# Performance work log

Measured on AMD Instinct MI355X. Metric: run time of the kernel, lower is better.

## Reference

```python
import jax, jax.numpy as jnp
import numpy as np

NPOINT, RADIUS, SIGMA, K = 1024, 0.1, 0.05, 32
KDE_K = 128  # N_points default of kernel_density_estimation_ball


def setup_inputs() -> dict:
    key = jax.random.key(0)
    ks = jax.random.split(key, 9)
    B, N, C = 4, 4096, 16

    def glorot(k, shape):
        fan_in, fan_out = shape
        return jax.random.normal(k, shape, jnp.float32) * jnp.sqrt(2.0 / (fan_in + fan_out))

    return {
        'xyz': jax.random.uniform(ks[0], (B, N, 3), jnp.float32),      # unit cube
        'feature': jax.random.normal(ks[1], (B, N, C), jnp.float32),
        'w_mlp0': glorot(ks[2], (3 + C, 128)),
        'w_mlp1': glorot(ks[3], (128, 128)),
        'w_mlp2': glorot(ks[4], (128, 256)),
        'w_wn': glorot(ks[5], (3, 32)),
        'w_nl0': glorot(ks[6], (1, 16)),
        'w_nl1': glorot(ks[7], (16, 1)),
        'w_np': glorot(ks[8], (32, 256)),
    }


def _pdist2(a, b):
    # squared pairwise distances [B, M, N]
    return (jnp.sum(a * a, -1)[:, :, None] + jnp.sum(b * b, -1)[:, None, :]
            - 2.0 * jnp.einsum('bmd,bnd->bmn', a, b))


def _fps(xyz, npoint):
    # farthest point sampling, seeded at index 0 (matches CUDA op semantics)
    B, N, _ = xyz.shape

    def step(carry, _):
        min_d, last = carry
        p = jnp.take_along_axis(xyz, last[:, None, None], axis=1)  # [B,1,3]
        d = jnp.sum((xyz - p) ** 2, -1)                            # [B,N]
        min_d = jnp.minimum(min_d, d)
        nxt = jnp.argmax(min_d, axis=1).astype(jnp.int32)
        return (min_d, nxt), nxt

    init = (jnp.full((B, N), jnp.inf, xyz.dtype), jnp.zeros((B,), jnp.int32))
    _, rest = jax.lax.scan(step, init, None, length=npoint - 1)
    return jnp.concatenate([jnp.zeros((B, 1), jnp.int32), rest.T], axis=1)  # [B,npoint]


def _ball_query(xyz, radius, k):
    # first-k-in-index-order neighbors with d2 < r^2, padded with first hit
    B, N, _ = xyz.shape
    d2 = _pdist2(xyz, xyz)
    in_ball = d2 < radius * radius                 # self always included
    j = jnp.arange(N, dtype=jnp.int32)
    keys = jnp.where(in_ball, j, j + N)            # in-ball indices sort first
    _, idx = jax.lax.top_k(-keys, k)               # k smallest keys -> positions j
    cnt = jnp.minimum(jnp.sum(in_ball, axis=-1), k)            # [B,N]
    valid = jnp.arange(k) < cnt[..., None]
    idx = jnp.where(valid, idx, idx[..., :1])
    return idx, cnt


def _kde_ball(xyz, radius, sigma, kde_k):
    idx, cnt = _ball_query(xyz, radius, kde_k)     # [B,N,kde_k], [B,N]
    b_ix = jnp.arange(xyz.shape[0])[:, None, None]
    g = xyz[b_ix, idx] - xyz[:, :, None, :]        # [B,N,kde_k,3]
    R = jnp.sqrt(jnp.float32(sigma))
    quad = jnp.sum(jnp.square(g / R), axis=-1)     # [B,N,kde_k]
    mvn = jnp.exp(-0.5 * quad - 3.0 * jnp.log(R) - 1.5 * jnp.log(2.0 * 3.1415926))
    first = mvn[..., :1]
    total = jnp.sum(mvn, axis=-1, keepdims=True)
    cntf = cnt.astype(xyz.dtype)[..., None]
    total = total - first * (jnp.float32(kde_k) - cntf)  # remove padded duplicates
    return total / cntf                             # [B,N,1]


def _knn(k, src, q):
    d2 = _pdist2(q, src)                            # [B,P,N]
    _, idx = jax.lax.top_k(-d2, k)                  # ascending distance
    return idx


def _forward(xyz, feature, w_mlp0, w_mlp1, w_mlp2, w_wn, w_nl0, w_nl1, w_np):
    B = xyz.shape[0]
    conv = lambda x, w: jax.nn.relu(jnp.einsum('bpkc,cf->bpkf', x, w))  # bias-free 1x1 conv

    fps_idx = _fps(xyz, NPOINT)
    new_xyz = jnp.take_along_axis(xyz, fps_idx[..., None], axis=1)      # [B,P,3]

    knn_idx = _knn(K, xyz, new_xyz)                                      # [B,P,K]
    b_ix = jnp.arange(B)[:, None, None]
    grouped_xyz = xyz[b_ix, knn_idx] - new_xyz[:, :, None, :]            # [B,P,K,3]
    grouped_feature = jnp.concatenate([grouped_xyz, feature[b_ix, knn_idx]], axis=-1)

    inv_density = 1.0 / _kde_ball(xyz, RADIUS, SIGMA, KDE_K)             # [B,N,1]
    grouped_density = inv_density[b_ix, knn_idx]                          # [B,P,K,1]
    density_scale = grouped_density / jnp.max(grouped_density, axis=2, keepdims=True)

    h = conv(conv(conv(grouped_feature, w_mlp0), w_mlp1), w_mlp2)        # [B,P,K,256]
    weight = conv(grouped_xyz, w_wn)                                      # [B,P,K,32]
    density_scale = conv(conv(density_scale, w_nl0), w_nl1)               # [B,P,K,1]

    pts = h * density_scale
    pts = jnp.einsum('bpkc,bpkw->bpcw', pts, weight)                      # [B,P,256,32]
    # np_conv: 1x1 kernel with stride [1, mlp[-1]] + VALID -> only c=0 slice survives
    out = jax.nn.relu(jnp.einsum('bpw,wf->bpf', pts[:, :, 0, :], w_np))   # [B,P,256]
    return new_xyz, out


def reference(xyz, feature, w_mlp0, w_mlp1, w_mlp2, w_wn, w_nl0, w_nl1, w_np):
    return _forward(xyz, feature, w_mlp0, w_mlp1, w_mlp2, w_wn, w_nl0, w_nl1, w_np)
```

## Files before the change

### kernel.cpp

```cpp
#include <hip/hip_runtime.h>
#include <math.h>

#pragma clang fp contract(off)

typedef float v2f __attribute__((ext_vector_type(2)));

__global__ __launch_bounds__(256) void prep_kernel(
    const float* __restrict__ xyz, const float* __restrict__ w0,
    const float* __restrict__ w1, const float* __restrict__ w2,
    float* __restrict__ norms, float* __restrict__ W0T,
    float* __restrict__ W1T, float* __restrict__ W2c)
{
    int t = blockIdx.x * 256 + threadIdx.x;
    if (t < 16384) {
        float x = xyz[t*3+0], y = xyz[t*3+1], z = xyz[t*3+2];
        norms[t] = (x*x + y*y) + z*z;
        int c = t >> 7, k = t & 127;
        W1T[c*128 + k] = w1[k*128 + c];
    }
    if (t < 2432) { int c = t / 19, i = t - c*19; W0T[t] = w0[i*128 + c]; }
    if (t < 128)  { W2c[t] = w2[t*256]; }
}

template<int CTRL>
__device__ __forceinline__ unsigned long long dpp_u64(unsigned long long k) {
    int lo = (int)(unsigned int)k;
    int hi = (int)(unsigned int)(k >> 32);
    int plo = __builtin_amdgcn_update_dpp(lo, lo, CTRL, 0xF, 0xF, false);
    int phi = __builtin_amdgcn_update_dpp(hi, hi, CTRL, 0xF, 0xF, false);
    return ((unsigned long long)(unsigned int)phi << 32) | (unsigned int)plo;
}
template<int CTRL>
__device__ __forceinline__ unsigned long long max_u64_dpp(unsigned long long k) {
    unsigned long long p = dpp_u64<CTRL>(k);
    return p > k ? p : k;
}
template<int CTRL>
__device__ __forceinline__ unsigned long long min_u64_dpp(unsigned long long k) {
    unsigned long long p = dpp_u64<CTRL>(k);
    return p < k ? p : k;
}
__device__ __forceinline__ unsigned long long max_u64(unsigned long long a,
                                                      unsigned long long b) {
    return a > b ? a : b;
}

__global__ __launch_bounds__(512) void fps_kde_kernel(
    const float* __restrict__ xyz, const float* __restrict__ norms,
    float* __restrict__ new_xyz, float* __restrict__ invden)
{
    __shared__ float4 pts[4096];
    __shared__ float  nxb[3072];
    __shared__ __attribute__((aligned(16))) unsigned long long swk[2][32];
    int tid = threadIdx.x;

    if (blockIdx.x < 4) {
        int b = blockIdx.x;
        const float* Xb = xyz + b*12288;
        for (int t = tid; t < 4096; t += 512)
            pts[t] = make_float4(Xb[t*3+0], Xb[t*3+1], Xb[t*3+2], 0.0f);
        __syncthreads();
        float4 P[8];
#pragma unroll
        for (int k = 0; k < 8; ++k) P[k] = pts[k*512 + tid];
        v2f Xp[4], Yp[4], Zp[4], md2[4];
#pragma unroll
        for (int k = 0; k < 4; ++k) {
            Xp[k].x = P[k].x;  Xp[k].y = P[k+4].x;
            Yp[k].x = P[k].y;  Yp[k].y = P[k+4].y;
            Zp[k].x = P[k].z;  Zp[k].y = P[k+4].z;
            md2[k].x = INFINITY; md2[k].y = INFINITY;
        }
        unsigned ip[8];
#pragma unroll
        for (int k = 0; k < 8; ++k) ip[k] = ~((unsigned)(k*512 + tid));
        float cx = pts[0].x, cy = pts[0].y, cz = pts[0].z;
        if (tid == 0) { nxb[0] = cx; nxb[1] = cy; nxb[2] = cz; }
        int buf = 0;
        for (int it = 1; it < 1024; ++it) {
            v2f cx2, cy2, cz2;
            cx2.x = cx; cx2.y = cx;
            cy2.x = cy; cy2.y = cy;
            cz2.x = cz; cz2.y = cz;
#pragma unroll
            for (int k = 0; k < 4; ++k) {
                v2f dx = Xp[k] - cx2, dy = Yp[k] - cy2, dz = Zp[k] - cz2;
                v2f dd = (dx*dx + dy*dy) + dz*dz;
                md2[k].x = fminf(md2[k].x, dd.x);
                md2[k].y = fminf(md2[k].y, dd.y);
            }
            unsigned long long k0 =
                ((unsigned long long)__float_as_uint(md2[0].x) << 32) | ip[0];
            unsigned long long k1 =
                ((unsigned long long)__float_as_uint(md2[1].x) << 32) | ip[1];
            unsigned long long k2 =
                ((unsigned long long)__float_as_uint(md2[2].x) << 32) | ip[2];
            unsigned long long k3 =
                ((unsigned long long)__float_as_uint(md2[3].x) << 32) | ip[3];
            unsigned long long k4 =
                ((unsigned long long)__float_as_uint(md2[0].y) << 32) | ip[4];
            unsigned long long k5 =
                ((unsigned long long)__float_as_uint(md2[1].y) << 32) | ip[5];
            unsigned long long k6 =
                ((unsigned long long)__float_as_uint(md2[2].y) << 32) | ip[6];
            unsigned long long k7 =
                ((unsigned long long)__float_as_uint(md2[3].y) << 32) | ip[7];
            unsigned long long t01 = max_u64(k0, k1);
            unsigned long long t23 = max_u64(k2, k3);
            unsigned long long t45 = max_u64(k4, k5);
            unsigned long long t67 = max_u64(k6, k7);
            unsigned long long t03 = max_u64(t01, t23);
            unsigned long long t47 = max_u64(t45, t67);
            unsigned long long key = max_u64(t03, t47);
            key = max_u64_dpp<0xB1>(key);
            key = max_u64_dpp<0x4E>(key);
            key = max_u64_dpp<0x141>(key);
            key = max_u64_dpp<0x140>(key);
            if ((tid & 15) == 0) swk[buf][tid >> 4] = key;
            __syncthreads();
            uint4 w4 = *((const uint4*)&swk[buf][(tid & 15) << 1]);
            unsigned long long kA = ((unsigned long long)w4.y << 32) | w4.x;
            unsigned long long kB = ((unsigned long long)w4.w << 32) | w4.z;
            unsigned long long kk = kA > kB ? kA : kB;
            kk = max_u64_dpp<0xB1>(kk);
            kk = max_u64_dpp<0x4E>(kk);
            kk = max_u64_dpp<0x141>(kk);
            kk = max_u64_dpp<0x140>(kk);
            int fp = (int)(~(unsigned int)kk);
            float4 c = pts[fp];
            cx = c.x; cy = c.y; cz = c.z;
            if (tid == 0) { nxb[it*3+0] = cx; nxb[it*3+1] = cy; nxb[it*3+2] = cz; }
            buf ^= 1;
        }
        __syncthreads();
        float* NX = new_xyz + b*3072;
        for (int t = tid; t < 3072; t += 512) NX[t] = nxb[t];
    } else {
        int idx = blockIdx.x - 4;
        int b = idx >> 9;
        int wave = tid >> 6, lane = tid & 63;
        int i_local = ((idx & 511) << 3) + wave;
        const float* Xb = xyz + b*12288;
        const float* Nb = norms + b*4096;
        for (int t = tid; t < 4096; t += 512)
            pts[t] = make_float4(Xb[t*3+0], Xb[t*3+1], Xb[t*3+2], Nb[t]);
        __syncthreads();
        float4 c = pts[i_local];
        const float Rv    = sqrtf(0.05f);
        const float inv_s = 1.0f / (Rv*Rv);
        const float K1    = -3.0f*logf(Rv) - 1.5f*logf(2.0f*3.1415926f);
        float csum = 0.0f; int cnt = 0;
        for (int j = lane; j < 4096; j += 64) {
            float4 q = pts[j];
            float dot = (c.x*q.x + c.y*q.y) + c.z*q.z;
            float t2 = 2.0f * dot;
            float d2 = (c.w + q.w) - t2;
            if (d2 < 0.01f) {
                float gx = q.x - c.x, gy = q.y - c.y, gz = q.z - c.z;
                float dd = (gx*gx + gy*gy) + gz*gz;
                csum += expf(-0.5f * (dd * inv_s) + K1);
                cnt  += 1;
            }
        }
#pragma unroll
        for (int m = 1; m < 64; m <<= 1) {
            csum += __shfl_xor(csum, m, 64);
            cnt  += __shfl_xor(cnt,  m, 64);
        }
        if (lane == 0) {
            float den = csum / (float)cnt;
            invden[b*4096 + i_local] = 1.0f / den;
        }
    }
}

__global__ __launch_bounds__(256) void knn_kernel(
    const float* __restrict__ xyz, const float* __restrict__ norms,
    const float* __restrict__ new_xyz, int* __restrict__ knn_idx)
{
    __shared__ unsigned sd2[4*4096];
    __shared__ int sIdx[4*32];
    int wave = threadIdx.x >> 6, lane = threadIdx.x & 63;
    int qg = blockIdx.x*4 + wave;
    int b = qg >> 10;
    const float* Q = new_xyz + qg*3;
    float qx = Q[0], qy = Q[1], qz = Q[2];
    float nq = (qx*qx + qy*qy) + qz*qz;
    const float* Xb = xyz + b*12288;
    const float* Nb = norms + b*4096;
    unsigned* d2w = sd2 + wave*4096;
    for (int j = lane; j < 4096; j += 64) {
        float x = Xb[j*3+0], y = Xb[j*3+1], z = Xb[j*3+2];
        float dot = (qx*x + qy*y) + qz*z;
        float t2 = 2.0f*dot;
        float d = (nq + Nb[j]) - t2;
        unsigned u = __float_as_uint(d);
        unsigned m = ((unsigned)((int)u >> 31)) | 0x80000000u;
        d2w[j] = u ^ m;
    }
    for (int r = 0; r < 32; ++r) {
        unsigned best = 0xFFFFFFFFu; int bj = 0;
#pragma unroll
        for (int t = 0; t < 16; ++t) {
            int jb = t*256 + lane*4;
            uint4 v = *((const uint4*)(d2w + jb));
            if (v.x < best) { best = v.x; bj = jb;   }
            if (v.y < best) { best = v.y; bj = jb+1; }
            if (v.z < best) { best = v.z; bj = jb+2; }
            if (v.w < best) { best = v.w; bj = jb+3; }
        }
        unsigned long long key = ((unsigned long long)best << 32) | (unsigned)bj;
        key = min_u64_dpp<0xB1>(key);
        key = min_u64_dpp<0x4E>(key);
        key = min_u64_dpp<0x141>(key);
        key = min_u64_dpp<0x140>(key);
        key = min_u64_dpp<0x142>(key);
        key = min_u64_dpp<0x143>(key);
        int jwin = __builtin_amdgcn_readlane((int)(unsigned)key, 63);
        if (lane == 0) { sIdx[wave*32 + r] = jwin; d2w[jwin] = 0xFFFFFFFFu; }
    }
    if (lane < 32) knn_idx[qg*32 + lane] = sIdx[wave*32 + lane];
}

__global__ __launch_bounds__(256, 2) void group_mlp_kernel(
    const float* __restrict__ xyz, const float* __restrict__ feat,
    const float* __restrict__ new_xyz, const int* __restrict__ knn_idx,
    const float* __restrict__ invden,
    const float* __restrict__ W0T, const float* __restrict__ W1T,
    const float* __restrict__ W2c, const float* __restrict__ wwn,
    const float* __restrict__ wnl0, const float* __restrict__ wnl1,
    float* __restrict__ ptsw)
{
    int row = blockIdx.x*256 + threadIdx.x;
    int k  = row & 31;
    int pg = row >> 5;
    int b  = row >> 15;
    int j  = knn_idx[row];
    const float* Xb = xyz + b*12288;
    const float* Q  = new_xyz + pg*3;
    float in[19];
    in[0] = Xb[j*3+0] - Q[0];
    in[1] = Xb[j*3+1] - Q[1];
    in[2] = Xb[j*3+2] - Q[2];
    const float4* F = (const float4*)(feat + (size_t)(b*4096 + j)*16);
    float4 f0 = F[0], f1 = F[1], f2 = F[2], f3 = F[3];
    in[3]=f0.x; in[4]=f0.y; in[5]=f0.z; in[6]=f0.w;
    in[7]=f1.x; in[8]=f1.y; in[9]=f1.z; in[10]=f1.w;
    in[11]=f2.x; in[12]=f2.y; in[13]=f2.z; in[14]=f2.w;
    in[15]=f3.x; in[16]=f3.y; in[17]=f3.z; in[18]=f3.w;

    float gd = invden[b*4096 + j];
    float mx = gd;
#pragma unroll
    for (int m = 1; m < 32; m <<= 1) mx = fmaxf(mx, __shfl_xor(mx, m, 64));
    float dsc = gd / mx;
    float sacc = 0.0f;
#pragma unroll
    for (int t = 0; t < 16; ++t)
        sacc = fmaf(fmaxf(dsc * wnl0[t], 0.0f), wnl1[t], sacc);
    float ds = fmaxf(sacc, 0.0f);

    float h1[128];
#pragma unroll
    for (int c = 0; c < 128; ++c) {
        const float* w = W0T + c*19;
        float a = in[0]*w[0];
#pragma unroll
        for (int i = 1; i < 19; ++i) a = fmaf(in[i], w[i], a);
        h1[c] = fmaxf(a, 0.0f);
    }
    float acc0 = 0.0f;
    for (int c2 = 0; c2 < 128; ++c2) {
        const float* w = W1T + c2*128;
        float a0 = 0.0f, a1 = 0.0f, a2 = 0.0f, a3 = 0.0f;
#pragma unroll
        for (int kk = 0; kk < 128; kk += 4) {
            a0 = fmaf(h1[kk+0], w[kk+0], a0);
            a1 = fmaf(h1[kk+1], w[kk+1], a1);
            a2 = fmaf(h1[kk+2], w[kk+2], a2);
            a3 = fmaf(h1[kk+3], w[kk+3], a3);
        }
        float a = (a0+a1) + (a2+a3);
        acc0 = fmaf(fmaxf(a, 0.0f), W2c[c2], acc0);
    }
    float h0 = fmaxf(acc0, 0.0f);
    float s = h0 * ds;

    float gx = in[0], gy = in[1], gz = in[2];
    float* pw = ptsw + pg*32;
#pragma unroll
    for (int w = 0; w < 32; ++w) {
        float a = gx * wwn[w];
        a = fmaf(gy, wwn[32+w], a);
        a = fmaf(gz, wwn[64+w], a);
        float part = s * fmaxf(a, 0.0f);
#pragma unroll
        for (int m = 1; m < 32; m <<= 1) part += __shfl_xor(part, m, 64);
        if (k == 0) pw[w] = part;
    }
}

__global__ __launch_bounds__(256) void final_kernel(
    const float* __restrict__ ptsw, const float* __restrict__ wnp,
    float* __restrict__ out)
{
    int pg = blockIdx.x;
    int f  = threadIdx.x;
    const float* pw = ptsw + pg*32;
    float a = 0.0f;
#pragma unroll
    for (int w = 0; w < 32; ++w) a = fmaf(pw[w], wnp[w*256+f], a);
    out[pg*256 + f] = fmaxf(a, 0.0f);
}

extern "C" void kernel_launch(void* const* d_in, const int* in_sizes, int n_in,
                              void* d_out, int out_size, void* d_ws, size_t ws_size,
                              hipStream_t stream) {
    const float* xyz  = (const float*)d_in[0];
    const float* feat = (const float*)d_in[1];
    const float* w0   = (const float*)d_in[2];
    const float* w1   = (const float*)d_in[3];
    const float* w2   = (const float*)d_in[4];
    const float* wwn  = (const float*)d_in[5];
    const float* wnl0 = (const float*)d_in[6];
    const float* wnl1 = (const float*)d_in[7];
    const float* wnp  = (const float*)d_in[8];

    float* out_all  = (float*)d_out;
    float* new_xyz  = out_all;
    float* out2     = out_all + 12288;

    char* ws = (char*)d_ws;
    float* norms  = (float*)(ws + 0);
    float* invden = (float*)(ws + 65536);
    int*   knn    = (int*)  (ws + 131072);
    float* ptsw   = (float*)(ws + 655360);
    float* W0T    = (float*)(ws + 1179648);
    float* W1T    = (float*)(ws + 1189376);
    float* W2c    = (float*)(ws + 1254912);

    prep_kernel<<<64, 256, 0, stream>>>(xyz, w0, w1, w2, norms, W0T, W1T, W2c);
    fps_kde_kernel<<<2052, 512, 0, stream>>>(xyz, norms, new_xyz, invden);
    knn_kernel<<<1024, 256, 0, stream>>>(xyz, norms, new_xyz, knn);
    group_mlp_kernel<<<512, 256, 0, stream>>>(xyz, feat, new_xyz, knn, invden,
                                              W0T, W1T, W2c, wwn, wnl0, wnl1, ptsw);
    final_kernel<<<4096, 256, 0, stream>>>(ptsw, wnp, out2);
}
```

Measured before the change: 950.0 us.

## Run FPS on four waves with full-wave DPP reduction and a four-entry LDS combine

The farthest-point-sampling blocks now run the selection loop on 256 threads (four waves) instead of 512. Each thread handles 16 points instead of 8. The argmax key is reduced across the whole wave with the row_bcast DPP steps, so only four wave results go to shared memory and every thread reads them back with two vector loads, replacing the second DPP reduction over 32 partials. The idle upper threads only match the barriers. This cuts barrier participants and cross-wave reduction latency on the serial 1023-iteration critical path, at the cost of more distance work per thread.

```diff
diff --git a/kernel.cpp b/kernel.cpp
--- a/kernel.cpp
+++ b/kernel.cpp
@@ -51,7 +51,7 @@
 {
     __shared__ float4 pts[4096];
     __shared__ float  nxb[3072];
-    __shared__ __attribute__((aligned(16))) unsigned long long swk[2][32];
+    __shared__ __attribute__((aligned(16))) unsigned long long swk[2][4];
     int tid = threadIdx.x;
 
     if (blockIdx.x < 4) {
@@ -60,77 +60,80 @@
         for (int t = tid; t < 4096; t += 512)
             pts[t] = make_float4(Xb[t*3+0], Xb[t*3+1], Xb[t*3+2], 0.0f);
         __syncthreads();
-        float4 P[8];
-#pragma unroll
-        for (int k = 0; k < 8; ++k) P[k] = pts[k*512 + tid];
-        v2f Xp[4], Yp[4], Zp[4], md2[4];
-#pragma unroll
-        for (int k = 0; k < 4; ++k) {
-            Xp[k].x = P[k].x;  Xp[k].y = P[k+4].x;
-            Yp[k].x = P[k].y;  Yp[k].y = P[k+4].y;
-            Zp[k].x = P[k].z;  Zp[k].y = P[k+4].z;
-            md2[k].x = INFINITY; md2[k].y = INFINITY;
-        }
-        unsigned ip[8];
-#pragma unroll
-        for (int k = 0; k < 8; ++k) ip[k] = ~((unsigned)(k*512 + tid));
-        float cx = pts[0].x, cy = pts[0].y, cz = pts[0].z;
-        if (tid == 0) { nxb[0] = cx; nxb[1] = cy; nxb[2] = cz; }
-        int buf = 0;
-        for (int it = 1; it < 1024; ++it) {
-            v2f cx2, cy2, cz2;
-            cx2.x = cx; cx2.y = cx;
-            cy2.x = cy; cy2.y = cy;
-            cz2.x = cz; cz2.y = cz;
-#pragma unroll
-            for (int k = 0; k < 4; ++k) {
-                v2f dx = Xp[k] - cx2, dy = Yp[k] - cy2, dz = Zp[k] - cz2;
-                v2f dd = (dx*dx + dy*dy) + dz*dz;
-                md2[k].x = fminf(md2[k].x, dd.x);
-                md2[k].y = fminf(md2[k].y, dd.y);
+        if (tid < 256) {
+            int lane = tid & 63, wave = tid >> 6;
+            v2f Xp[8], Yp[8], Zp[8], md2[8];
+            unsigned ip[16];
+#pragma unroll
+            for (int k = 0; k < 8; ++k) {
+                float4 A = pts[(2*k)*256 + tid];
+                float4 B = pts[(2*k+1)*256 + tid];
+                Xp[k].x = A.x;  Xp[k].y = B.x;
+                Yp[k].x = A.y;  Yp[k].y = B.y;
+                Zp[k].x = A.z;  Zp[k].y = B.z;
+                md2[k].x = INFINITY; md2[k].y = INFINITY;
+                ip[2*k]   = ~((unsigned)((2*k)*256 + tid));
+                ip[2*k+1] = ~((unsigned)((2*k+1)*256 + tid));
             }
-            unsigned long long k0 =
-                ((unsigned long long)__float_as_uint(md2[0].x) << 32) | ip[0];
-            unsigned long long k1 =
-                ((unsigned long long)__float_as_uint(md2[1].x) << 32) | ip[1];
-            unsigned long long k2 =
-                ((unsigned long long)__float_as_uint(md2[2].x) << 32) | ip[2];
-            unsigned long long k3 =
-                ((unsigned long long)__float_as_uint(md2[3].x) << 32) | ip[3];
-            unsigned long long k4 =
-                ((unsigned long long)__float_as_uint(md2[0].y) << 32) | ip[4];
-            unsigned long long k5 =
-                ((unsigned long long)__float_as_uint(md2[1].y) << 32) | ip[5];
-            unsigned long long k6 =
-                ((unsigned long long)__float_as_uint(md2[2].y) << 32) | ip[6];
-            unsigned long long k7 =
-                ((unsigned long long)__float_as_uint(md2[3].y) << 32) | ip[7];
-            unsigned long long t01 = max_u64(k0, k1);
-            unsigned long long t23 = max_u64(k2, k3);
-            unsigned long long t45 = max_u64(k4, k5);
-            unsigned long long t67 = max_u64(k6, k7);
-            unsigned long long t03 = max_u64(t01, t23);
-            unsigned long long t47 = max_u64(t45, t67);
-            unsigned long long key = max_u64(t03, t47);
-            key = max_u64_dpp<0xB1>(key);
-            key = max_u64_dpp<0x4E>(key);
-            key = max_u64_dpp<0x141>(key);
-            key = max_u64_dpp<0x140>(key);
-            if ((tid & 15) == 0) swk[buf][tid >> 4] = key;
-            __syncthreads();
-            uint4 w4 = *((const uint4*)&swk[buf][(tid & 15) << 1]);
-            unsigned long long kA = ((unsigned long long)w4.y << 32) | w4.x;
-            unsigned long long kB = ((unsigned long long)w4.w << 32) | w4.z;
-            unsigned long long kk = kA > kB ? kA : kB;
-            kk = max_u64_dpp<0xB1>(kk);
-            kk = max_u64_dpp<0x4E>(kk);
-            kk = max_u64_dpp<0x141>(kk);
-            kk = max_u64_dpp<0x140>(kk);
-            int fp = (int)(~(unsigned int)kk);
-            float4 c = pts[fp];
-            cx = c.x; cy = c.y; cz = c.z;
-            if (tid == 0) { nxb[it*3+0] = cx; nxb[it*3+1] = cy; nxb[it*3+2] = cz; }
-            buf ^= 1;
+            float cx = pts[0].x, cy = pts[0].y, cz = pts[0].z;
+            if (tid == 0) { nxb[0] = cx; nxb[1] = cy; nxb[2] = cz; }
+            int buf = 0;
+            for (int it = 1; it < 1024; ++it) {
+                v2f cx2, cy2, cz2;
+                cx2.x = cx; cx2.y = cx;
+                cy2.x = cy; cy2.y = cy;
+                cz2.x = cz; cz2.y = cz;
+#pragma unroll
+                for (int k = 0; k < 8; ++k) {
+                    v2f dx = Xp[k] - cx2, dy = Yp[k] - cy2, dz = Zp[k] - cz2;
+                    v2f dd = (dx*dx + dy*dy) + dz*dz;
+                    md2[k].x = fminf(md2[k].x, dd.x);
+                    md2[k].y = fminf(md2[k].y, dd.y);
+                }
+                unsigned long long m0 = max_u64(
+                    max_u64(((unsigned long long)__float_as_uint(md2[0].x) << 32) | ip[0],
+                            ((unsigned long long)__float_as_uint(md2[0].y) << 32) | ip[1]),
+                    max_u64(((unsigned long long)__float_as_uint(md2[1].x) << 32) | ip[2],
+                            ((unsigned long long)__float_as_uint(md2[1].y) << 32) | ip[3]));
+                unsigned long long m1 = max_u64(
+                    max_u64(((unsigned long long)__float_as_uint(md2[2].x) << 32) | ip[4],
+                            ((unsigned long long)__float_as_uint(md2[2].y) << 32) | ip[5]),
+                    max_u64(((unsigned long long)__float_as_uint(md2[3].x) << 32) | ip[6],
+                            ((unsigned long long)__float_as_uint(md2[3].y) << 32) | ip[7]));
+                unsigned long long m2 = max_u64(
+                    max_u64(((unsigned long long)__float_as_uint(md2[4].x) << 32) | ip[8],
+                            ((unsigned long long)__float_as_uint(md2[4].y) << 32) | ip[9]),
+                    max_u64(((unsigned long long)__float_as_uint(md2[5].x) << 32) | ip[10],
+                            ((unsigned long long)__float_as_uint(md2[5].y) << 32) | ip[11]));
+                unsigned long long m3 = max_u64(
+                    max_u64(((unsigned long long)__float_as_uint(md2[6].x) << 32) | ip[12],
+                            ((unsigned long long)__float_as_uint(md2[6].y) << 32) | ip[13]),
+                    max_u64(((unsigned long long)__float_as_uint(md2[7].x) << 32) | ip[14],
+                            ((unsigned long long)__float_as_uint(md2[7].y) << 32) | ip[15]));
+                unsigned long long key = max_u64(max_u64(m0, m1), max_u64(m2, m3));
+                key = max_u64_dpp<0xB1>(key);
+                key = max_u64_dpp<0x4E>(key);
+                key = max_u64_dpp<0x141>(key);
+                key = max_u64_dpp<0x140>(key);
+                key = max_u64_dpp<0x142>(key);
+                key = max_u64_dpp<0x143>(key);
+                if (lane == 63) swk[buf][wave] = key;
+                __syncthreads();
+                const uint4* s4 = (const uint4*)&swk[buf][0];
+                uint4 wa = s4[0], wb = s4[1];
+                unsigned long long kA = ((unsigned long long)wa.y << 32) | wa.x;
+                unsigned long long kB = ((unsigned long long)wa.w << 32) | wa.z;
+                unsigned long long kC = ((unsigned long long)wb.y << 32) | wb.x;
+                unsigned long long kD = ((unsigned long long)wb.w << 32) | wb.z;
+                unsigned long long kk = max_u64(max_u64(kA, kB), max_u64(kC, kD));
+                int fp = (int)(~(unsigned int)kk);
+                float4 c = pts[fp];
+                cx = c.x; cy = c.y; cz = c.z;
+                if (tid == 0) { nxb[it*3+0] = cx; nxb[it*3+1] = cy; nxb[it*3+2] = cz; }
+                buf ^= 1;
+            }
+        } else {
+            for (int it = 1; it < 1024; ++it) __syncthreads();
         }
         __syncthreads();
         float* NX = new_xyz + b*3072;
```

Measured after the change: 924.0 us. 1.03x faster.
